# Kernel optimization log

Hardware: AMD Instinct MI355X
Metric: run time of the kernel (lower is better)

## Reference

```python
import jax, jax.numpy as jnp
import numpy as np

N, E, R, B, DIN, H1, H2 = 50000, 1000000, 8, 30, 64, 64, 64


def setup_inputs() -> dict:
    key = jax.random.key(0)
    ks = jax.random.split(key, 12)
    node_features = jax.random.normal(ks[0], (N, DIN), dtype=jnp.float32)
    src = jax.random.randint(ks[1], (E,), 0, N)
    dst = jax.random.randint(ks[2], (E,), 0, N)
    edge_index = jnp.stack([src, dst]).astype(jnp.int64)
    edge_norm = jax.random.uniform(ks[3], (E,), dtype=jnp.float32)
    edge_type = jax.random.randint(ks[4], (E,), 0, R).astype(jnp.int64)
    s = 0.05  # param init scale
    basis = jax.random.normal(ks[5], (B, DIN, H1), dtype=jnp.float32) * s
    comp = jax.random.normal(ks[6], (R, B), dtype=jnp.float32) * s
    loop_weight = jax.random.normal(ks[7], (DIN, H1), dtype=jnp.float32) * s
    bias1 = jnp.zeros((H1,), dtype=jnp.float32)
    weight2 = jax.random.normal(ks[8], (H1, H2), dtype=jnp.float32) * s
    bias2 = jnp.zeros((H2,), dtype=jnp.float32)
    return dict(node_features=node_features, edge_index=edge_index,
                edge_norm=edge_norm, edge_type=edge_type, basis=basis,
                comp=comp, loop_weight=loop_weight, bias1=bias1,
                weight2=weight2, bias2=bias2)


def reference(node_features, edge_index, edge_norm, edge_type, basis, comp,
              loop_weight, bias1, weight2, bias2):
    n = node_features.shape[0]
    src, dst = edge_index[0], edge_index[1]

    # ---- RGCNConv (basis decomposition, sum aggregation, self-loop, bias) ----
    # relation weights from bases: [R, DIN, H1]
    Wrel = jnp.einsum('rb,bio->rio', comp, basis)
    # transform every node by every relation once: [N, R, H1]
    xr = jnp.einsum('ni,rio->nro', node_features, Wrel)
    # per-edge message via (src, edge_type) gather: [E, H1]
    msg = xr[src, edge_type]
    agg1 = jax.ops.segment_sum(msg, dst, num_segments=n)
    h = agg1 + node_features @ loop_weight + bias1

    # ---- GraphConv (symmetric 'both' normalization) ----
    ones = jnp.ones((src.shape[0],), dtype=h.dtype)
    deg_out = jnp.clip(jax.ops.segment_sum(ones, src, num_segments=n), 1.0, None)
    deg_in = jnp.clip(jax.ops.segment_sum(ones, dst, num_segments=n), 1.0, None)
    hs = h * jax.lax.rsqrt(deg_out)[:, None]
    agg2 = jax.ops.segment_sum(hs[src], dst, num_segments=n)
    agg2 = agg2 * jax.lax.rsqrt(deg_in)[:, None]
    out = agg2 @ weight2 + bias2
    return out
```

## Files before the change

### kernel.cpp

```cpp
#include <hip/hip_runtime.h>

#define N_NODES 50000
#define N_EDGES 1000000
#define NB      128
#define CHUNK   7813
#define NQ      8
#define QN      6256
#define NBLK2   196

#define A_PART    0
#define A_XR      0
#define A_DEGP    115200000
#define A_ROWPTR  115400000
#define A_BSUM    115600128
#define A_BBASE   115601024
#define A_CSR     115601920
#define A_HS      123601920
#define A_WALL    136401920

typedef unsigned int uint32;

__global__ void k_wall(const float* __restrict__ comp, const float* __restrict__ basis,
                       const float* __restrict__ loopw, float* __restrict__ Wall) {
    int idx = blockIdx.x * 256 + threadIdx.x;
    if (idx >= 9 * 4096) return;
    int r = idx >> 12, io = idx & 4095;
    float acc;
    if (r < 8) {
        acc = 0.f;
        #pragma unroll
        for (int b = 0; b < 30; ++b) acc += comp[r * 30 + b] * basis[b * 4096 + io];
    } else {
        acc = loopw[io];
    }
    Wall[idx] = acc;
}

__global__ __launch_bounds__(256) void k_hist2(const int* __restrict__ ei,
                                               uint32* __restrict__ part) {
    __shared__ __align__(16) uint32 h[QN];
    int t = threadIdx.x, b = blockIdx.x, q = blockIdx.y;
    int lo = q * QN;
    int nq = N_NODES - lo; if (nq > QN) nq = QN;
    int4* h4 = (int4*)h;
    for (int i = t; i < QN / 4; i += 256) h4[i] = make_int4(0, 0, 0, 0);
    __syncthreads();
    int e0 = b * CHUNK, e1 = e0 + CHUNK;
    if (e1 > N_EDGES) e1 = N_EDGES;
    for (int e = e0 + t; e < e1; e += 256) {
        int s = ei[e], d = ei[N_EDGES + e];
        unsigned rs = (unsigned)(s - lo), rd = (unsigned)(d - lo);
        if (rs < (unsigned)QN) atomicAdd(&h[rs], 1u);
        if (rd < (unsigned)QN) atomicAdd(&h[rd], 0x10000u);
    }
    __syncthreads();
    int4* d4 = (int4*)(part + b * N_NODES + lo);
    const int4* s4 = (const int4*)h;
    for (int i = t; i < nq / 4; i += 256) d4[i] = s4[i];
}

__global__ __launch_bounds__(256) void k_merge(const uint32* __restrict__ part,
                                               uint32* __restrict__ degp,
                                               int* __restrict__ bsum) {
    int t = threadIdx.x, v = blockIdx.x * 256 + t;
    uint32 s = 0;
    if (v < N_NODES) {
        #pragma unroll 8
        for (int b = 0; b < NB; ++b) s += part[b * N_NODES + v];
        degp[v] = s;
    }
    int din = (int)(s >> 16);
    int r = din;
    #pragma unroll
    for (int d = 1; d < 64; d <<= 1) r += __shfl_xor(r, d);
    __shared__ int wsum[4];
    int lane = t & 63, wid = t >> 6;
    if (lane == 0) wsum[wid] = r;
    __syncthreads();
    if (t == 0) bsum[blockIdx.x] = wsum[0] + wsum[1] + wsum[2] + wsum[3];
}

__global__ void k_scanb(const int* __restrict__ bsum, int* __restrict__ bbase) {
    int t = threadIdx.x;
    int v = (t < NBLK2) ? bsum[t] : 0;
    int lane = t & 63, wid = t >> 6;
    int x = v;
    #pragma unroll
    for (int d = 1; d < 64; d <<= 1) {
        int y = __shfl_up(x, d);
        if (lane >= d) x += y;
    }
    __shared__ int wsum[4];
    if (lane == 63) wsum[wid] = x;
    __syncthreads();
    int base = 0;
    for (int w = 0; w < wid; ++w) base += wsum[w];
    if (t < NBLK2) bbase[t] = base + x - v;
}

__global__ __launch_bounds__(256) void k_base(uint32* __restrict__ part,
                                              const uint32* __restrict__ degp,
                                              const int* __restrict__ bbase,
                                              int* __restrict__ rowptr) {
    int t = threadIdx.x, v = blockIdx.x * 256 + t;
    int din = (v < N_NODES) ? (int)(degp[v] >> 16) : 0;
    int lane = t & 63, wid = t >> 6;
    int x = din;
    #pragma unroll
    for (int d = 1; d < 64; d <<= 1) {
        int y = __shfl_up(x, d);
        if (lane >= d) x += y;
    }
    __shared__ int wsum[4];
    if (lane == 63) wsum[wid] = x;
    __syncthreads();
    int base = bbase[blockIdx.x];
    for (int w = 0; w < wid; ++w) base += wsum[w];
    int start = base + x - din;
    if (v < N_NODES) {
        rowptr[v] = start;
        if (v == N_NODES - 1) rowptr[N_NODES] = start + din;
        uint32 run = (uint32)start;
        for (int b = 0; b < NB; ++b) {
            uint32 p = part[b * N_NODES + v];
            part[b * N_NODES + v] = run;
            run += (p >> 16);
        }
    }
}

__global__ __launch_bounds__(256) void k_fill2(const int* __restrict__ ei,
                                               const int* __restrict__ etype,
                                               const uint32* __restrict__ fillbase,
                                               int2* __restrict__ csr) {
    __shared__ __align__(16) uint32 cur[QN];
    int t = threadIdx.x, b = blockIdx.x, q = blockIdx.y;
    int lo = q * QN;
    int nq = N_NODES - lo; if (nq > QN) nq = QN;
    const int4* s4 = (const int4*)(fillbase + b * N_NODES + lo);
    int4* c4 = (int4*)cur;
    for (int i = t; i < nq / 4; i += 256) c4[i] = s4[i];
    __syncthreads();
    int e0 = b * CHUNK, e1 = e0 + CHUNK;
    if (e1 > N_EDGES) e1 = N_EDGES;
    for (int e = e0 + t; e < e1; e += 256) {
        int d = ei[N_EDGES + e];
        unsigned rd = (unsigned)(d - lo);
        if (rd < (unsigned)QN) {
            int s = ei[e], ty = etype[e];
            uint32 pos = atomicAdd(&cur[rd], 1u);
            csr[pos] = make_int2(s * 9 + ty, s);
        }
    }
}

__global__ __launch_bounds__(256) void k_xr(const float* __restrict__ x,
                                            const float* __restrict__ Wall,
                                            float* __restrict__ xr) {
    __shared__ __align__(16) float At[64 * 68];
    __shared__ __align__(16) float Wt[64 * 64];
    int t = threadIdx.x;
    int n0 = blockIdx.x * 64;
    int r = blockIdx.y;
    #pragma unroll
    for (int j = 0; j < 16; ++j) {
        int f = t + j * 256;
        int n = f >> 6, k = f & 63;
        float v = (n0 + n < N_NODES) ? x[(n0 + n) * 64 + k] : 0.f;
        At[k * 68 + n] = v;
    }
    #pragma unroll
    for (int j = 0; j < 16; ++j) {
        int f = t + j * 256;
        Wt[f] = Wall[r * 4096 + f];
    }
    __syncthreads();
    int cg = t & 15, rg = t >> 4;
    float acc[4][4];
    #pragma unroll
    for (int i = 0; i < 4; ++i)
        #pragma unroll
        for (int j = 0; j < 4; ++j) acc[i][j] = 0.f;
    #pragma unroll 4
    for (int k = 0; k < 64; ++k) {
        float4 a = *(const float4*)&At[k * 68 + 4 * rg];
        float4 w = *(const float4*)&Wt[k * 64 + 4 * cg];
        acc[0][0] += a.x * w.x; acc[0][1] += a.x * w.y; acc[0][2] += a.x * w.z; acc[0][3] += a.x * w.w;
        acc[1][0] += a.y * w.x; acc[1][1] += a.y * w.y; acc[1][2] += a.y * w.z; acc[1][3] += a.y * w.w;
        acc[2][0] += a.z * w.x; acc[2][1] += a.z * w.y; acc[2][2] += a.z * w.z; acc[2][3] += a.z * w.w;
        acc[3][0] += a.w * w.x; acc[3][1] += a.w * w.y; acc[3][2] += a.w * w.z; acc[3][3] += a.w * w.w;
    }
    #pragma unroll
    for (int i = 0; i < 4; ++i) {
        int n = n0 + 4 * rg + i;
        if (n < N_NODES) {
            float4 o = make_float4(acc[i][0], acc[i][1], acc[i][2], acc[i][3]);
            *(float4*)&xr[n * 576 + r * 64 + 4 * cg] = o;
        }
    }
}

__global__ __launch_bounds__(256) void k_agg1(const float* __restrict__ xr,
                                              const int2* __restrict__ csr,
                                              const int* __restrict__ rowptr,
                                              const uint32* __restrict__ degp,
                                              const float* __restrict__ bias1,
                                              float* __restrict__ hs) {
    int wid = threadIdx.x >> 6, lane = threadIdx.x & 63;
    int v = blockIdx.x * 4 + wid;
    if (v >= N_NODES) return;
    float acc = xr[(v * 9 + 8) * 64 + lane] + bias1[lane];
    int j = rowptr[v], end = rowptr[v + 1];
    for (; j + 4 <= end; j += 4) {
        int r0 = csr[j].x, r1 = csr[j + 1].x, r2 = csr[j + 2].x, r3 = csr[j + 3].x;
        float a0 = xr[r0 * 64 + lane], a1 = xr[r1 * 64 + lane];
        float a2 = xr[r2 * 64 + lane], a3 = xr[r3 * 64 + lane];
        acc += a0; acc += a1; acc += a2; acc += a3;
    }
    for (; j < end; ++j) acc += xr[csr[j].x * 64 + lane];
    float dg = (float)(degp[v] & 0xffffu);
    if (dg < 1.f) dg = 1.f;
    hs[v * 64 + lane] = acc * rsqrtf(dg);
}

__global__ __launch_bounds__(256) void k_layer2(const float* __restrict__ hs,
                                                const int2* __restrict__ csr,
                                                const int* __restrict__ rowptr,
                                                const uint32* __restrict__ degp,
                                                const float* __restrict__ w2,
                                                const float* __restrict__ bias2,
                                                float* __restrict__ out) {
    __shared__ __align__(16) float W2s[64 * 64];
    __shared__ __align__(16) float ys[4 * 64];
    int t = threadIdx.x;
    #pragma unroll
    for (int j = 0; j < 16; ++j) W2s[t + j * 256] = w2[t + j * 256];
    int wid = t >> 6, lane = t & 63;
    int v = blockIdx.x * 4 + wid;
    float acc = 0.f;
    int j = 0, end = 0;
    if (v < N_NODES) { j = rowptr[v]; end = rowptr[v + 1]; }
    for (; j + 4 <= end; j += 4) {
        int r0 = csr[j].y, r1 = csr[j + 1].y, r2 = csr[j + 2].y, r3 = csr[j + 3].y;
        float a0 = hs[r0 * 64 + lane], a1 = hs[r1 * 64 + lane];
        float a2 = hs[r2 * 64 + lane], a3 = hs[r3 * 64 + lane];
        acc += a0; acc += a1; acc += a2; acc += a3;
    }
    for (; j < end; ++j) acc += hs[csr[j].y * 64 + lane];
    if (v < N_NODES) {
        float dg = (float)(degp[v] >> 16);
        if (dg < 1.f) dg = 1.f;
        ys[wid * 64 + lane] = acc * rsqrtf(dg);
    }
    __syncthreads();
    if (v >= N_NODES) return;
    float o = bias2[lane];
    const float* yrow = &ys[wid * 64];
    #pragma unroll 4
    for (int k = 0; k < 64; ++k) o += yrow[k] * W2s[k * 64 + lane];
    out[v * 64 + lane] = o;
}

extern "C" void kernel_launch(void* const* d_in, const int* in_sizes, int n_in,
                              void* d_out, int out_size, void* d_ws, size_t ws_size,
                              hipStream_t stream) {
    const float* x      = (const float*)d_in[0];
    const int*   ei     = (const int*)d_in[1];
    const int*   etype  = (const int*)d_in[3];
    const float* basis  = (const float*)d_in[4];
    const float* comp   = (const float*)d_in[5];
    const float* loopw  = (const float*)d_in[6];
    const float* bias1  = (const float*)d_in[7];
    const float* w2     = (const float*)d_in[8];
    const float* bias2  = (const float*)d_in[9];
    float* out = (float*)d_out;

    char* ws = (char*)d_ws;
    uint32* part   = (uint32*)(ws + A_PART);
    float*  xr     = (float*)(ws + A_XR);
    uint32* degp   = (uint32*)(ws + A_DEGP);
    int*    rowptr = (int*)(ws + A_ROWPTR);
    int*    bsum   = (int*)(ws + A_BSUM);
    int*    bbase  = (int*)(ws + A_BBASE);
    int2*   csr    = (int2*)(ws + A_CSR);
    float*  hs     = (float*)(ws + A_HS);
    float*  Wall   = (float*)(ws + A_WALL);

    k_wall<<<144, 256, 0, stream>>>(comp, basis, loopw, Wall);
    k_hist2<<<dim3(NB, NQ), 256, 0, stream>>>(ei, part);
    k_merge<<<NBLK2, 256, 0, stream>>>(part, degp, bsum);
    k_scanb<<<1, 256, 0, stream>>>(bsum, bbase);
    k_base<<<NBLK2, 256, 0, stream>>>(part, degp, bbase, rowptr);
    k_fill2<<<dim3(NB, NQ), 256, 0, stream>>>(ei, etype, part, csr);
    k_xr<<<dim3((N_NODES + 63) / 64, 9), 256, 0, stream>>>(x, Wall, xr);
    k_agg1<<<N_NODES / 4, 256, 0, stream>>>(xr, csr, rowptr, degp, bias1, hs);
    k_layer2<<<N_NODES / 4, 256, 0, stream>>>(hs, csr, rowptr, degp, w2, bias2, out);
}
```

Measured before the change: 317.2 us.

## Aggregate raw features per relation before transform, replacing per-relation node transform

Reorders layer 1 so each destination first sums the raw 64-wide source features into eight per-relation buckets plus its own features, and only then multiplies that 576-wide vector by the stacked relation and loop weights. This replaces the transform of every node by all nine weight matrices and the gathers from the 576-wide transformed table with gathers from the 64-wide input, so the gathered working set is much smaller and cache-friendlier. In exchange, the per-edge accumulation switches on relation type with a wave-uniform readfirstlane, and a new register-blocked GEMM reads A rows straight from global memory without shared-memory tiling.

```diff
diff --git a/kernel.cpp b/kernel.cpp
--- a/kernel.cpp
+++ b/kernel.cpp
@@ -9,7 +9,7 @@
 #define NBLK2   196
 
 #define A_PART    0
-#define A_XR      0
+#define A_AGG     0
 #define A_DEGP    115200000
 #define A_ROWPTR  115400000
 #define A_BSUM    115600128
@@ -149,78 +149,110 @@
         if (rd < (unsigned)QN) {
             int s = ei[e], ty = etype[e];
             uint32 pos = atomicAdd(&cur[rd], 1u);
-            csr[pos] = make_int2(s * 9 + ty, s);
+            csr[pos] = make_int2(s, ty);
         }
     }
 }
 
-__global__ __launch_bounds__(256) void k_xr(const float* __restrict__ x,
-                                            const float* __restrict__ Wall,
-                                            float* __restrict__ xr) {
-    __shared__ __align__(16) float At[64 * 68];
-    __shared__ __align__(16) float Wt[64 * 64];
-    int t = threadIdx.x;
-    int n0 = blockIdx.x * 64;
-    int r = blockIdx.y;
-    #pragma unroll
-    for (int j = 0; j < 16; ++j) {
-        int f = t + j * 256;
-        int n = f >> 6, k = f & 63;
-        float v = (n0 + n < N_NODES) ? x[(n0 + n) * 64 + k] : 0.f;
-        At[k * 68 + n] = v;
-    }
-    #pragma unroll
-    for (int j = 0; j < 16; ++j) {
-        int f = t + j * 256;
-        Wt[f] = Wall[r * 4096 + f];
-    }
-    __syncthreads();
-    int cg = t & 15, rg = t >> 4;
-    float acc[4][4];
-    #pragma unroll
-    for (int i = 0; i < 4; ++i)
-        #pragma unroll
-        for (int j = 0; j < 4; ++j) acc[i][j] = 0.f;
-    #pragma unroll 4
-    for (int k = 0; k < 64; ++k) {
-        float4 a = *(const float4*)&At[k * 68 + 4 * rg];
-        float4 w = *(const float4*)&Wt[k * 64 + 4 * cg];
-        acc[0][0] += a.x * w.x; acc[0][1] += a.x * w.y; acc[0][2] += a.x * w.z; acc[0][3] += a.x * w.w;
-        acc[1][0] += a.y * w.x; acc[1][1] += a.y * w.y; acc[1][2] += a.y * w.z; acc[1][3] += a.y * w.w;
-        acc[2][0] += a.z * w.x; acc[2][1] += a.z * w.y; acc[2][2] += a.z * w.z; acc[2][3] += a.z * w.w;
-        acc[3][0] += a.w * w.x; acc[3][1] += a.w * w.y; acc[3][2] += a.w * w.z; acc[3][3] += a.w * w.w;
-    }
-    #pragma unroll
-    for (int i = 0; i < 4; ++i) {
-        int n = n0 + 4 * rg + i;
-        if (n < N_NODES) {
-            float4 o = make_float4(acc[i][0], acc[i][1], acc[i][2], acc[i][3]);
-            *(float4*)&xr[n * 576 + r * 64 + 4 * cg] = o;
-        }
-    }
-}
-
-__global__ __launch_bounds__(256) void k_agg1(const float* __restrict__ xr,
-                                              const int2* __restrict__ csr,
-                                              const int* __restrict__ rowptr,
-                                              const uint32* __restrict__ degp,
-                                              const float* __restrict__ bias1,
-                                              float* __restrict__ hs) {
+__global__ __launch_bounds__(256) void k_gather1(const float* __restrict__ x,
+                                                 const int2* __restrict__ csr,
+                                                 const int* __restrict__ rowptr,
+                                                 float* __restrict__ agg) {
     int wid = threadIdx.x >> 6, lane = threadIdx.x & 63;
     int v = blockIdx.x * 4 + wid;
     if (v >= N_NODES) return;
-    float acc = xr[(v * 9 + 8) * 64 + lane] + bias1[lane];
+    float a0 = 0.f, a1 = 0.f, a2 = 0.f, a3 = 0.f;
+    float a4 = 0.f, a5 = 0.f, a6 = 0.f, a7 = 0.f;
+#define ACCUM(VAL, TY) { int sty = __builtin_amdgcn_readfirstlane(TY); \
+    switch (sty) { \
+        case 0: a0 += (VAL); break; case 1: a1 += (VAL); break; \
+        case 2: a2 += (VAL); break; case 3: a3 += (VAL); break; \
+        case 4: a4 += (VAL); break; case 5: a5 += (VAL); break; \
+        case 6: a6 += (VAL); break; default: a7 += (VAL); break; } }
     int j = rowptr[v], end = rowptr[v + 1];
     for (; j + 4 <= end; j += 4) {
-        int r0 = csr[j].x, r1 = csr[j + 1].x, r2 = csr[j + 2].x, r3 = csr[j + 3].x;
-        float a0 = xr[r0 * 64 + lane], a1 = xr[r1 * 64 + lane];
-        float a2 = xr[r2 * 64 + lane], a3 = xr[r3 * 64 + lane];
-        acc += a0; acc += a1; acc += a2; acc += a3;
-    }
-    for (; j < end; ++j) acc += xr[csr[j].x * 64 + lane];
-    float dg = (float)(degp[v] & 0xffffu);
-    if (dg < 1.f) dg = 1.f;
-    hs[v * 64 + lane] = acc * rsqrtf(dg);
+        int2 e0 = csr[j], e1 = csr[j + 1], e2 = csr[j + 2], e3 = csr[j + 3];
+        float v0 = x[e0.x * 64 + lane], v1 = x[e1.x * 64 + lane];
+        float v2 = x[e2.x * 64 + lane], v3 = x[e3.x * 64 + lane];
+        ACCUM(v0, e0.y); ACCUM(v1, e1.y); ACCUM(v2, e2.y); ACCUM(v3, e3.y);
+    }
+    for (; j < end; ++j) {
+        int2 e = csr[j];
+        float val = x[e.x * 64 + lane];
+        ACCUM(val, e.y);
+    }
+#undef ACCUM
+    float* o = agg + (size_t)v * 576 + lane;
+    o[0]   = a0; o[64]  = a1; o[128] = a2; o[192] = a3;
+    o[256] = a4; o[320] = a5; o[384] = a6; o[448] = a7;
+    o[512] = x[v * 64 + lane];
+}
+
+__global__ __launch_bounds__(256) void k_gemm576(const float* __restrict__ agg,
+                                                 const float* __restrict__ Wall,
+                                                 const uint32* __restrict__ degp,
+                                                 const float* __restrict__ bias1,
+                                                 float* __restrict__ hs) {
+    int t = threadIdx.x;
+    int wave = t >> 6, lane = t & 63;
+    int ng = lane >> 3, cg = lane & 7;
+    int nbase = (blockIdx.x * 4 + wave) * 32 + ng * 4;
+    int c0 = cg * 8;
+    int n0 = nbase + 0; if (n0 > N_NODES - 1) n0 = N_NODES - 1;
+    int n1 = nbase + 1; if (n1 > N_NODES - 1) n1 = N_NODES - 1;
+    int n2 = nbase + 2; if (n2 > N_NODES - 1) n2 = N_NODES - 1;
+    int n3 = nbase + 3; if (n3 > N_NODES - 1) n3 = N_NODES - 1;
+    const float* A0 = agg + (size_t)n0 * 576;
+    const float* A1 = agg + (size_t)n1 * 576;
+    const float* A2 = agg + (size_t)n2 * 576;
+    const float* A3 = agg + (size_t)n3 * 576;
+    const float* B = Wall + c0;
+    float acc[4][8];
+    #pragma unroll
+    for (int i = 0; i < 4; ++i)
+        #pragma unroll
+        for (int c = 0; c < 8; ++c) acc[i][c] = 0.f;
+    for (int k = 0; k < 576; k += 4) {
+        float4 va0 = *(const float4*)(A0 + k);
+        float4 va1 = *(const float4*)(A1 + k);
+        float4 va2 = *(const float4*)(A2 + k);
+        float4 va3 = *(const float4*)(A3 + k);
+        #pragma unroll
+        for (int kk = 0; kk < 4; ++kk) {
+            float4 bl = *(const float4*)(B + (k + kk) * 64);
+            float4 bh = *(const float4*)(B + (k + kk) * 64 + 4);
+            float w0 = ((const float*)&va0)[kk];
+            float w1 = ((const float*)&va1)[kk];
+            float w2 = ((const float*)&va2)[kk];
+            float w3 = ((const float*)&va3)[kk];
+            acc[0][0] += w0 * bl.x; acc[0][1] += w0 * bl.y; acc[0][2] += w0 * bl.z; acc[0][3] += w0 * bl.w;
+            acc[0][4] += w0 * bh.x; acc[0][5] += w0 * bh.y; acc[0][6] += w0 * bh.z; acc[0][7] += w0 * bh.w;
+            acc[1][0] += w1 * bl.x; acc[1][1] += w1 * bl.y; acc[1][2] += w1 * bl.z; acc[1][3] += w1 * bl.w;
+            acc[1][4] += w1 * bh.x; acc[1][5] += w1 * bh.y; acc[1][6] += w1 * bh.z; acc[1][7] += w1 * bh.w;
+            acc[2][0] += w2 * bl.x; acc[2][1] += w2 * bl.y; acc[2][2] += w2 * bl.z; acc[2][3] += w2 * bl.w;
+            acc[2][4] += w2 * bh.x; acc[2][5] += w2 * bh.y; acc[2][6] += w2 * bh.z; acc[2][7] += w2 * bh.w;
+            acc[3][0] += w3 * bl.x; acc[3][1] += w3 * bl.y; acc[3][2] += w3 * bl.z; acc[3][3] += w3 * bl.w;
+            acc[3][4] += w3 * bh.x; acc[3][5] += w3 * bh.y; acc[3][6] += w3 * bh.z; acc[3][7] += w3 * bh.w;
+        }
+    }
+    float4 b1l = *(const float4*)(bias1 + c0);
+    float4 b1h = *(const float4*)(bias1 + c0 + 4);
+    #pragma unroll
+    for (int i = 0; i < 4; ++i) {
+        int n = nbase + i;
+        if (n < N_NODES) {
+            float dg = (float)(degp[n] & 0xffffu);
+            if (dg < 1.f) dg = 1.f;
+            float rs = rsqrtf(dg);
+            float4 o1, o2;
+            o1.x = (acc[i][0] + b1l.x) * rs; o1.y = (acc[i][1] + b1l.y) * rs;
+            o1.z = (acc[i][2] + b1l.z) * rs; o1.w = (acc[i][3] + b1l.w) * rs;
+            o2.x = (acc[i][4] + b1h.x) * rs; o2.y = (acc[i][5] + b1h.y) * rs;
+            o2.z = (acc[i][6] + b1h.z) * rs; o2.w = (acc[i][7] + b1h.w) * rs;
+            *(float4*)(hs + (size_t)n * 64 + c0) = o1;
+            *(float4*)(hs + (size_t)n * 64 + c0 + 4) = o2;
+        }
+    }
 }
 
 __global__ __launch_bounds__(256) void k_layer2(const float* __restrict__ hs,
@@ -241,12 +273,12 @@
     int j = 0, end = 0;
     if (v < N_NODES) { j = rowptr[v]; end = rowptr[v + 1]; }
     for (; j + 4 <= end; j += 4) {
-        int r0 = csr[j].y, r1 = csr[j + 1].y, r2 = csr[j + 2].y, r3 = csr[j + 3].y;
+        int r0 = csr[j].x, r1 = csr[j + 1].x, r2 = csr[j + 2].x, r3 = csr[j + 3].x;
         float a0 = hs[r0 * 64 + lane], a1 = hs[r1 * 64 + lane];
         float a2 = hs[r2 * 64 + lane], a3 = hs[r3 * 64 + lane];
         acc += a0; acc += a1; acc += a2; acc += a3;
     }
-    for (; j < end; ++j) acc += hs[csr[j].y * 64 + lane];
+    for (; j < end; ++j) acc += hs[csr[j].x * 64 + lane];
     if (v < N_NODES) {
         float dg = (float)(degp[v] >> 16);
         if (dg < 1.f) dg = 1.f;
@@ -277,7 +309,7 @@
 
     char* ws = (char*)d_ws;
     uint32* part   = (uint32*)(ws + A_PART);
-    float*  xr     = (float*)(ws + A_XR);
+    float*  agg    = (float*)(ws + A_AGG);
     uint32* degp   = (uint32*)(ws + A_DEGP);
     int*    rowptr = (int*)(ws + A_ROWPTR);
     int*    bsum   = (int*)(ws + A_BSUM);
@@ -292,7 +324,7 @@
     k_scanb<<<1, 256, 0, stream>>>(bsum, bbase);
     k_base<<<NBLK2, 256, 0, stream>>>(part, degp, bbase, rowptr);
     k_fill2<<<dim3(NB, NQ), 256, 0, stream>>>(ei, etype, part, csr);
-    k_xr<<<dim3((N_NODES + 63) / 64, 9), 256, 0, stream>>>(x, Wall, xr);
-    k_agg1<<<N_NODES / 4, 256, 0, stream>>>(xr, csr, rowptr, degp, bias1, hs);
+    k_gather1<<<N_NODES / 4, 256, 0, stream>>>(x, csr, rowptr, agg);
+    k_gemm576<<<(N_NODES + 127) / 128, 256, 0, stream>>>(agg, Wall, degp, bias1, hs);
     k_layer2<<<N_NODES / 4, 256, 0, stream>>>(hs, csr, rowptr, degp, w2, bias2, out);
 }
```

New measurement: 425.3 us. 34.1% more time.
